# Kernel tuning notes

Measured on AMD Instinct MI355X. Metric: run time of the kernel, lower is better.

## Reference

```python
import jax, jax.numpy as jnp
import numpy as np

B, S, D = 32, 257, 1024
H, HD = 16, 64
E, R, K = 8, 16, 2
SCALE = HD ** -0.5


def _lora_linear(x, w_fixed, A_all, B_all, bias, idx, gates):
    # x: [B,S,D]; w_fixed: [O,D]; A_all: [E,R,D]; B_all: [E,O,R]; idx: [B,K]; gates: [B,K]
    base = jnp.einsum('bsd,od->bso', x, w_fixed)
    A_sel = A_all[idx]  # [B,K,R,D] per-sample expert gather
    B_sel = B_all[idx]  # [B,K,O,R]
    xa = jnp.einsum('bsd,bkrd->bksr', x, A_sel)          # low-rank down-proj
    expert = jnp.einsum('bksr,bkor,bk->bso', xa, B_sel, gates)
    return base + expert + bias


def setup_inputs() -> dict:
    key = jax.random.key(0)
    ks = jax.random.split(key, 20)
    inp = {
        'hidden_states': jax.random.normal(ks[0], (B, S, D), jnp.float32),
        'top_k_indices': jax.random.randint(ks[1], (B, K), 0, E),
        'top_k_gates': jax.random.uniform(ks[2], (B, K), jnp.float32),
    }
    i = 3
    for name in ('q', 'k', 'v', 'o'):
        inp[f'w{name}_fixed'] = jax.random.normal(ks[i], (D, D), jnp.float32) * 0.02; i += 1
        inp[f'A_{name}'] = jax.random.normal(ks[i], (E, R, D), jnp.float32) * 0.02; i += 1
        inp[f'B_{name}'] = jax.random.normal(ks[i], (E, D, R), jnp.float32) * 0.02; i += 1
        inp[f'b_{name}'] = jnp.zeros((D,), jnp.float32)
    return inp


def reference(hidden_states, top_k_indices, top_k_gates,
              wq_fixed, A_q, B_q, b_q,
              wk_fixed, A_k, B_k, b_k,
              wv_fixed, A_v, B_v, b_v,
              wo_fixed, A_o, B_o, b_o):
    idx, gates = top_k_indices, top_k_gates
    q = _lora_linear(hidden_states, wq_fixed, A_q, B_q, b_q, idx, gates) * SCALE
    k = _lora_linear(hidden_states, wk_fixed, A_k, B_k, b_k, idx, gates)
    v = _lora_linear(hidden_states, wv_fixed, A_v, B_v, b_v, idx, gates)
    # [B,S,D] -> [B,H,S,HD]
    q = q.reshape(B, S, H, HD).transpose(0, 2, 1, 3)
    k = k.reshape(B, S, H, HD).transpose(0, 2, 1, 3)
    v = v.reshape(B, S, H, HD).transpose(0, 2, 1, 3)
    attn = jax.nn.softmax(jnp.einsum('bhsd,bhtd->bhst', q, k), axis=-1)
    out = jnp.einsum('bhst,bhtd->bhsd', attn, v)
    out = out.transpose(0, 2, 1, 3).reshape(B, S, D)
    return _lora_linear(out, wo_fixed, A_o, B_o, b_o, idx, gates)
```

## Files before the change

kernel.cpp:

```cpp
#include <hip/hip_runtime.h>


#define BB 32
#define SS 257
#define DD 1024
#define HH 16
#define HDIM 64
#define EE 8
#define RR 16
#define MTOT (BB * SS)
#define MPAD 8448
#define VTS 264

typedef __attribute__((ext_vector_type(8))) _Float16 f16x8;
typedef __attribute__((ext_vector_type(4))) float f32x4;

static __device__ __forceinline__ float4 ld4(const float* p) {
    return *(const float4*)p;
}
static __device__ __forceinline__ unsigned short f16b(float x) {
    union { _Float16 f; unsigned short u; } cv;
    cv.f = (_Float16)x;
    return cv.u;
}

static __device__ __forceinline__ void gl_lds16(const unsigned short* g,
                                                unsigned short* l) {
    __builtin_amdgcn_global_load_lds(
        (const __attribute__((address_space(1))) unsigned int*)g,
        (__attribute__((address_space(3))) unsigned int*)l, 16, 0, 0);
}

static __device__ __forceinline__ int xcd_swz(int orig, int nwg) {
    const int xcd = orig & 7;
    const int lin = orig >> 3;
    const int q = nwg >> 3;
    const int r = nwg & 7;
    return (xcd < r ? xcd * (q + 1) : r * (q + 1) + (xcd - r) * q) + lin;
}

__global__ __launch_bounds__(256) void prep(
    const float* __restrict__ hidden, const float* __restrict__ wq,
    const float* __restrict__ wk, const float* __restrict__ wv,
    const float* __restrict__ wo, const float* __restrict__ Aq,
    const float* __restrict__ Ak, const float* __restrict__ Av,
    const float* __restrict__ Ao, const float* __restrict__ Bq,
    const float* __restrict__ Bk, const float* __restrict__ Bv,
    const float* __restrict__ Bo, const int* __restrict__ tki,
    const float* __restrict__ tkg, unsigned short* __restrict__ Xf,
    unsigned short* __restrict__ Wcat, unsigned short* __restrict__ Who,
    unsigned short* __restrict__ A3, unsigned short* __restrict__ Ao16,
    unsigned short* __restrict__ Bccat, unsigned short* __restrict__ Bco)
{
    const int tid = threadIdx.x;
    int bx = blockIdx.x;
    if (bx < 8448) {
        long i = ((long)bx * 256 + tid) * 4;
        float4 v = (i < (long)MTOT * DD) ? ld4(&hidden[i])
                                         : make_float4(0.f, 0.f, 0.f, 0.f);
        ushort4 hv;
        hv.x = f16b(v.x); hv.y = f16b(v.y); hv.z = f16b(v.z); hv.w = f16b(v.w);
        *(ushort4*)&Xf[i] = hv;
        return;
    }
    bx -= 8448;
    if (bx < 4096) {
        const int sel = bx >> 10;
        long i = ((long)(bx & 1023) * 256 + tid) * 4;
        const float* src = (sel == 0) ? wq : (sel == 1) ? wk
                                          : (sel == 2) ? wv : wo;
        unsigned short* dst =
            (sel < 3) ? Wcat + (size_t)sel * DD * DD : Who;
        float4 v = ld4(&src[i]);
        ushort4 hv;
        hv.x = f16b(v.x); hv.y = f16b(v.y); hv.z = f16b(v.z); hv.w = f16b(v.w);
        *(ushort4*)&dst[i] = hv;
        return;
    }
    bx -= 4096;
    if (bx < 512) {
        const int sel = bx >> 7;
        long i = ((long)(bx & 127) * 256 + tid) * 4;
        const float* src = (sel == 0) ? Aq : (sel == 1) ? Ak
                                          : (sel == 2) ? Av : Ao;
        unsigned short* dst =
            (sel < 3) ? A3 + (size_t)sel * EE * RR * DD : Ao16;
        float4 v = ld4(&src[i]);
        ushort4 hv;
        hv.x = f16b(v.x); hv.y = f16b(v.y); hv.z = f16b(v.z); hv.w = f16b(v.w);
        *(ushort4*)&dst[i] = hv;
        return;
    }
    bx -= 512;
    {
        const int set = bx >> 8;
        const int i = (bx & 255) * 256 + tid;
        const int b = i >> 11;
        const int rem = i & 2047;
        const int n = rem >> 1;
        const int ke = rem & 1;
        const float* Ball = (set == 0) ? Bq : (set == 1) ? Bk
                                           : (set == 2) ? Bv : Bo;
        const int e = tki[b * 2 + ke];
        const float g = tkg[b * 2 + ke];
        const float* sp = &Ball[((size_t)e * DD + n) * RR];
        unsigned short o16[16];
#pragma unroll
        for (int r4 = 0; r4 < 4; ++r4) {
            float4 v = ld4(sp + r4 * 4);
            o16[r4 * 4 + 0] = f16b(g * v.x);
            o16[r4 * 4 + 1] = f16b(g * v.y);
            o16[r4 * 4 + 2] = f16b(g * v.z);
            o16[r4 * 4 + 3] = f16b(g * v.w);
        }
        unsigned short* dst =
            (set < 3) ? &Bccat[((size_t)b * 3072 + set * 1024 + n) * 32 + ke * 16]
                      : &Bco[((size_t)b * 1024 + n) * 32 + ke * 16];
        *(uint4*)&dst[0] = *(uint4*)&o16[0];
        *(uint4*)&dst[8] = *(uint4*)&o16[8];
    }
}

#define XA_STAGE(BUFI, KT)                                                     \
    do {                                                                       \
        unsigned short* base_ = Sx + (BUFI) * 8192;                            \
        const int k0_ = (KT) * 32;                                             \
        gl_lds16(Xf + xr0 + k0_, base_ + lbase);                               \
        gl_lds16(Xf + xr1 + k0_, base_ + 2048 + lbase);                        \
        gl_lds16(Ap + ar0 + k0_, base_ + 4096 + lbase);                        \
        gl_lds16(Ap + ar1 + k0_, base_ + 6144 + lbase);                        \
    } while (0)

#define XA_COMPUTE(BUFI)                                                       \
    do {                                                                       \
        const unsigned short* Ab_ = Sx + (BUFI) * 8192;                        \
        const unsigned short* Bb_ = Ab_ + 4096;                                \
        f16x8 af[4], bf[4];                                                    \
        const int sb = (quad ^ ((l16 >> 1) & 3)) * 8;                          \
        _Pragma("unroll") for (int t = 0; t < 4; ++t) {                        \
            af[t] = *(const f16x8*)&Ab_[(wm + t * 16 + l16) * 32 + sb];        \
            bf[t] = *(const f16x8*)&Bb_[(wn + t * 16 + l16) * 32 + sb];        \
        }                                                                      \
        _Pragma("unroll") for (int i = 0; i < 4; ++i)                          \
        _Pragma("unroll") for (int j = 0; j < 4; ++j)                          \
            acc[i][j] = __builtin_amdgcn_mfma_f32_16x16x32_f16(                \
                af[i], bf[j], acc[i][j], 0, 0, 0);                             \
    } while (0)

#define XA_SYNC() asm volatile("s_waitcnt vmcnt(0)\n\ts_barrier" ::: "memory")

__global__ __launch_bounds__(256) void gemm_xa(
    const unsigned short* __restrict__ Xf, const unsigned short* __restrict__ A0,
    const unsigned short* __restrict__ A1, const unsigned short* __restrict__ A2,
    unsigned short* __restrict__ XA, int ncols)
{
    __shared__ unsigned short Sx[16384];
    const int tid = threadIdx.x;
    const int m0 = blockIdx.y * 128;
    const int p = blockIdx.x;
    const unsigned short* Ap = (p == 0) ? A0 : (p == 1) ? A1 : A2;
    const int lane = tid & 63;
    const int w = tid >> 6;
    const int wm = (w >> 1) * 64;
    const int wn = (w & 1) * 64;
    const int l16 = lane & 15;
    const int quad = lane >> 4;

    f32x4 acc[4][4];
#pragma unroll
    for (int i = 0; i < 4; ++i)
#pragma unroll
        for (int j = 0; j < 4; ++j) acc[i][j] = (f32x4){0.f, 0.f, 0.f, 0.f};

    const int srow = tid >> 2;
    const int scol = (((tid & 3) ^ ((tid >> 3) & 3))) * 8;
    const int lbase = (tid & 192) * 8;
    const size_t xr0 = (size_t)(m0 + srow) * DD + scol;
    const size_t xr1 = (size_t)(m0 + srow + 64) * DD + scol;
    const size_t ar0 = (size_t)srow * DD + scol;
    const size_t ar1 = (size_t)(srow + 64) * DD + scol;

    XA_STAGE(0, 0);
#pragma unroll 1
    for (int kt = 0; kt < 32; ++kt) {
        XA_SYNC();
        if (kt < 31) XA_STAGE((kt + 1) & 1, kt + 1);
        XA_COMPUTE(kt & 1);
    }

#pragma unroll
    for (int j = 0; j < 4; ++j) {
        const int col = p * 128 + wn + j * 16 + l16;
#pragma unroll
        for (int i = 0; i < 4; ++i) {
            const int mb = m0 + wm + i * 16 + quad * 4;
#pragma unroll
            for (int rg = 0; rg < 4; ++rg) {
                const int m = mb + rg;
                if (m < MTOT)
                    XA[(size_t)m * ncols + col] = f16b(acc[i][j][rg]);
            }
        }
    }
}

#define QKV_STAGE(BUFI, KT)                                                    \
    do {                                                                       \
        unsigned short* dA_ = S + (BUFI) * 16384 + w * 512;                    \
        const int k0_ = (KT) * 32;                                             \
        gl_lds16(Xf + gA + k0_, dA_);                                          \
        gl_lds16(Wcat + gB + k0_, dA_ + 8192);                                 \
    } while (0)

#define QKV_PHASES(BUFI)                                                       \
    do {                                                                       \
        const unsigned short* Ab_ = S + (BUFI) * 16384;                        \
        const unsigned short* Bb_ = Ab_ + 8192;                                \
        f16x8 af_[4], bf_[4];                                                  \
        _Pragma("unroll") for (int j = 0; j < 4; ++j)                          \
            bf_[j] = *(const f16x8*)&Bb_[boff + j * 512];                      \
        _Pragma("unroll") for (int i = 0; i < 4; ++i)                          \
            af_[i] = *(const f16x8*)&Ab_[aoff + i * 512];                      \
        __builtin_amdgcn_s_setprio(1);                                         \
        _Pragma("unroll") for (int i = 0; i < 4; ++i)                          \
        _Pragma("unroll") for (int j = 0; j < 4; ++j)                          \
            acc[i][j] = __builtin_amdgcn_mfma_f32_16x16x32_f16(                \
                af_[i], bf_[j], acc[i][j], 0, 0, 0);                           \
        __builtin_amdgcn_s_setprio(0);                                         \
    } while (0)

#define QKV_SYNC() asm volatile("s_waitcnt vmcnt(0)\n\ts_barrier" ::: "memory")

__global__ __launch_bounds__(1024)
__attribute__((amdgpu_waves_per_eu(4, 8))) void gemm_qkv(
    const unsigned short* __restrict__ Xf, const unsigned short* __restrict__ Wcat,
    const float* __restrict__ bq, const float* __restrict__ bk,
    const float* __restrict__ bv, const unsigned short* __restrict__ XAd,
    const unsigned short* __restrict__ Bccat, const int* __restrict__ idx,
    unsigned short* __restrict__ qh, unsigned short* __restrict__ kh,
    unsigned short* __restrict__ vTg)
{
    __shared__ unsigned short S[32768];
    const int tid = threadIdx.x;
    const int wgid = xcd_swz(blockIdx.x, 396);
    const int bxn = wgid % 12;
    const int m0 = (wgid / 12) * 256;
    const int p = bxn >> 2;
    const int n0g = bxn * 256;
    const int nloc0 = (bxn & 3) * 256;
    const int lane = tid & 63;
    const int w = tid >> 6;
    const int wm = (w >> 2) * 64;
    const int wn = (w & 3) * 64;
    const int l16 = lane & 15;
    const int quad = lane >> 4;
    const int sb = (quad ^ ((l16 >> 1) & 3)) * 8;
    const int aoff = (wm + l16) * 32 + sb;
    const int boff = (wn + l16) * 32 + sb;

    f32x4 acc[4][4];
#pragma unroll
    for (int i = 0; i < 4; ++i)
#pragma unroll
        for (int j = 0; j < 4; ++j) acc[i][j] = (f32x4){0.f, 0.f, 0.f, 0.f};

    const int srow = tid >> 2;
    const int schk = ((tid & 3) ^ ((srow >> 1) & 3)) * 8;
    const size_t gA = (size_t)(m0 + srow) * DD + schk;
    const size_t gB = (size_t)(n0g + srow) * DD + schk;

    QKV_STAGE(0, 0);
#pragma unroll 1
    for (int kt = 0; kt < 32; ++kt) {
        QKV_SYNC();
        if (kt < 31) QKV_STAGE((kt + 1) & 1, kt + 1);
        QKV_PHASES(kt & 1);
    }

    {
        int m_hi = m0 + 255;
        if (m_hi >= MTOT) m_hi = MTOT - 1;
        const int b_first = m0 / SS;
        const int b_last = m_hi / SS;
        const int r = tid >> 2;
        const int cc = tid & 3;
        const int key = (r >> 1) & 3;
        const int g = cc ^ key;
        const uint4 z = make_uint4(0, 0, 0, 0);
#pragma unroll 1
        for (int bp = b_first; bp <= b_last; ++bp) {
            const int gm = m0 + r;
            const bool va = (gm < MTOT) && (gm / SS == bp);
            uint4 av = z;
            if (va) {
                const int e = idx[bp * 2 + (g >> 1)];
                av = *(const uint4*)&XAd[(size_t)gm * 384 + p * 128 +
                                         e * 16 + (g & 1) * 8];
            }
            const size_t bo = ((size_t)bp * 3072 + p * 1024 + nloc0 + r) * 32;
            uint4 bv2 = *(const uint4*)&Bccat[bo + g * 8];
            __syncthreads();
            *(uint4*)&S[r * 32 + cc * 8] = av;
            *(uint4*)&S[8192 + r * 32 + cc * 8] = bv2;
            __syncthreads();
            QKV_PHASES(0);
            __syncthreads();
        }
    }

    unsigned short* Epi = S;
    const float* bias = (p == 0) ? bq : (p == 1) ? bk : bv;
    if (p < 2) {
        const float alpha = (p == 0) ? 0.125f : 1.0f;
        unsigned short* C = (p == 0) ? qh : kh;
#pragma unroll 1
        for (int qtr = 0; qtr < 4; ++qtr) {
            if ((w >> 2) == qtr) {
#pragma unroll
                for (int j = 0; j < 4; ++j) {
                    const int col = wn + j * 16 + l16;
                    const float bvl = bias[nloc0 + col];
#pragma unroll
                    for (int i = 0; i < 4; ++i) {
                        const int ml = i * 16 + quad * 4;
#pragma unroll
                        for (int rg = 0; rg < 4; ++rg)
                            Epi[(ml + rg) * 264 + col] =
                                f16b(alpha * (acc[i][j][rg] + bvl));
                    }
                }
            }
            __syncthreads();
            {
                const int r = tid >> 4;
                const int c = (tid & 15) * 16;
                const int m = m0 + qtr * 64 + r;
                if (m < MTOT) {
#pragma unroll
                    for (int k = 0; k < 2; ++k)
                        *(uint4*)&C[(size_t)m * DD + nloc0 + c + k * 8] =
                            *(const uint4*)&Epi[r * 264 + c + k * 8];
                }
            }
            __syncthreads();
        }
    } else {
#pragma unroll 1
        for (int hh = 0; hh < 4; ++hh) {
            if ((w >> 2) == hh) {
#pragma unroll
                for (int j = 0; j < 4; ++j) {
                    const int col = wn + j * 16 + l16;
                    const float bvl = bias[nloc0 + col];
#pragma unroll
                    for (int i = 0; i < 4; ++i) {
                        const int ml = i * 16 + quad * 4;
                        ushort4 pk;
                        pk.x = f16b(acc[i][j][0] + bvl);
                        pk.y = f16b(acc[i][j][1] + bvl);
                        pk.z = f16b(acc[i][j][2] + bvl);
                        pk.w = f16b(acc[i][j][3] + bvl);
                        *(ushort4*)&Epi[col * 68 + ml] = pk;
                    }
                }
            }
            __syncthreads();
            {
                const int tl = tid & 63;
                const int mg = m0 + hh * 64 + tl;
                if (mg < MTOT) {
                    const int bq2 = mg / SS;
                    const int t = mg - bq2 * SS;
#pragma unroll 4
                    for (int k = 0; k < 16; ++k) {
                        const int nll = (tid >> 6) + k * 16;
                        const int d = nloc0 + nll;
                        vTg[((size_t)(bq2 * HH + (d >> 6)) * HDIM + (d & 63)) *
                                VTS + t] = Epi[nll * 68 + tl];
                    }
                }
            }
            __syncthreads();
        }
    }
}

#define O_STAGE(BUFI, KT)                                                      \
    do {                                                                       \
        unsigned short* b_ = S + (BUFI) * 12288;                               \
        const int k0_ = (KT) * 32;                                             \
        gl_lds16(Xf + gA1 + k0_, b_ + w * 1024);                               \
        gl_lds16(Xf + gA2 + k0_, b_ + w * 1024 + 512);                         \
        gl_lds16(Wh2 + gB + k0_, b_ + 8192 + w * 512);                         \
    } while (0)

#define O_PHASES(BUFI)                                                         \
    do {                                                                       \
        const unsigned short* Ab_ = S + (BUFI) * 12288;                        \
        const unsigned short* Bb_ = Ab_ + 8192;                                \
        f16x8 af_[4], bf_[4];                                                  \
        _Pragma("unroll") for (int j = 0; j < 4; ++j)                          \
            bf_[j] = *(const f16x8*)&Bb_[boff + j * 512];                      \
        _Pragma("unroll") for (int i = 0; i < 4; ++i)                          \
            af_[i] = *(const f16x8*)&Ab_[aoff + i * 512];                      \
        __builtin_amdgcn_s_setprio(1);                                         \
        _Pragma("unroll") for (int i = 0; i < 4; ++i)                          \
        _Pragma("unroll") for (int j = 0; j < 4; ++j)                          \
            acc[i][j] = __builtin_amdgcn_mfma_f32_16x16x32_f16(                \
                af_[i], bf_[j], acc[i][j], 0, 0, 0);                           \
        __builtin_amdgcn_s_setprio(0);                                         \
    } while (0)

__global__ __launch_bounds__(512)
__attribute__((amdgpu_waves_per_eu(2, 8))) void gemm_o(
    const unsigned short* __restrict__ Xf, const unsigned short* __restrict__ Wh2,
    const float* __restrict__ bias, const unsigned short* __restrict__ XAo,
    const unsigned short* __restrict__ Bco, const int* __restrict__ idx,
    float* __restrict__ Cf)
{
    __shared__ unsigned short S[24576];
    const int tid = threadIdx.x;
    const int wgid = xcd_swz(blockIdx.x, 264);
    const int m0 = (wgid >> 3) * 256;
    const int n0 = (wgid & 7) * 128;
    const int lane = tid & 63;
    const int w = tid >> 6;
    const int wm = (w >> 1) * 64;
    const int wn = (w & 1) * 64;
    const int l16 = lane & 15;
    const int quad = lane >> 4;
    const int sb = (quad ^ ((l16 >> 1) & 3)) * 8;
    const int aoff = (wm + l16) * 32 + sb;
    const int boff = (wn + l16) * 32 + sb;

    f32x4 acc[4][4];
#pragma unroll
    for (int i = 0; i < 4; ++i)
#pragma unroll
        for (int j = 0; j < 4; ++j) acc[i][j] = (f32x4){0.f, 0.f, 0.f, 0.f};

    const int rowA1 = w * 32 + (lane >> 2);
    const int chk = lane & 3;
    const int keyA = (rowA1 >> 1) & 3;
    const size_t gA1 = (size_t)(m0 + rowA1) * DD + (chk ^ keyA) * 8;
    const size_t gA2 = gA1 + (size_t)16 * DD;
    const int rowB = w * 16 + (lane >> 2);
    const int keyB = (rowB >> 1) & 3;
    const size_t gB = (size_t)(n0 + rowB) * DD + (chk ^ keyB) * 8;

    O_STAGE(0, 0);
#pragma unroll 1
    for (int kt = 0; kt < 32; ++kt) {
        QKV_SYNC();
        if (kt < 31) O_STAGE((kt + 1) & 1, kt + 1);
        O_PHASES(kt & 1);
    }

    {
        int m_hi = m0 + 255;
        if (m_hi >= MTOT) m_hi = MTOT - 1;
        const int b_first = m0 / SS;
        const int b_last = m_hi / SS;
        const int rA = tid >> 1;
        const int b0 = (tid & 1) * 2;
        const int keyTA = (rA >> 1) & 3;
        const int g0 = b0 ^ keyTA, g1 = (b0 + 1) ^ keyTA;
        const int rB = tid >> 2;
        const int ccB = tid & 3;
        const int gBt = ccB ^ ((rB >> 1) & 3);
        const uint4 z = make_uint4(0, 0, 0, 0);
#pragma unroll 1
        for (int bp = b_first; bp <= b_last; ++bp) {
            const int gm = m0 + rA;
            const bool va = (gm < MTOT) && (gm / SS == bp);
            uint4 av0 = z, av1 = z;
            if (va) {
                const int e0 = idx[bp * 2 + (g0 >> 1)];
                const int e1 = idx[bp * 2 + (g1 >> 1)];
                av0 = *(const uint4*)&XAo[(size_t)gm * 128 + e0 * 16 +
                                          (g0 & 1) * 8];
                av1 = *(const uint4*)&XAo[(size_t)gm * 128 + e1 * 16 +
                                          (g1 & 1) * 8];
            }
            const size_t bo = ((size_t)bp * 1024 + n0 + rB) * 32;
            uint4 bv2 = *(const uint4*)&Bco[bo + gBt * 8];
            __syncthreads();
            *(uint4*)&S[rA * 32 + b0 * 8] = av0;
            *(uint4*)&S[rA * 32 + (b0 + 1) * 8] = av1;
            *(uint4*)&S[8192 + rB * 32 + ccB * 8] = bv2;
            __syncthreads();
            O_PHASES(0);
            __syncthreads();
        }
    }

#pragma unroll
    for (int j = 0; j < 4; ++j) {
        const int n = n0 + wn + j * 16 + l16;
        const float bvl = bias[n];
#pragma unroll
        for (int i = 0; i < 4; ++i) {
            const int mb = m0 + wm + i * 16 + quad * 4;
#pragma unroll
            for (int rg = 0; rg < 4; ++rg) {
                const int m = mb + rg;
                if (m < MTOT) Cf[(size_t)m * DD + n] = acc[i][j][rg] + bvl;
            }
        }
    }
}

__global__ __launch_bounds__(512, 1) void attn_v4(
    const unsigned short* __restrict__ qh, const unsigned short* __restrict__ kh,
    const unsigned short* __restrict__ vT, unsigned short* __restrict__ Xf)
{
    __shared__ unsigned short Ks[288 * 64];
    __shared__ unsigned short Vt[64 * VTS];
    __shared__ unsigned short Qs[64 * 64];
    __shared__ unsigned short Ps[64 * 296];
    __shared__ float sredm[2][64];
    __shared__ float sreds[2][64];

    const int tid = threadIdx.x;
    const int h = blockIdx.x, b = blockIdx.y;
    const int cb = h * HDIM;
    const int lane = tid & 63;
    const int w = tid >> 6;
    const int r0 = (w & 3) * 16;
    const int ch = w >> 2;
    const int l16 = lane & 15;
    const int quad = lane >> 4;

    const size_t kbase = (size_t)(b * SS) * DD + cb;
    {
        const int rr = w * 8 + (lane >> 3);
        const int cg = ((lane & 7) ^ (rr & 7)) * 8;
#pragma unroll
        for (int c = 0; c < 4; ++c)
            gl_lds16(kh + kbase + (size_t)(c * 64 + rr) * DD + cg,
                     &Ks[(c * 64 + w * 8) * 64]);
    }
    if (tid < 256) {
        uint4 z = make_uint4(0, 0, 0, 0);
        if (tid < 8) z = *(const uint4*)&kh[kbase + (size_t)256 * DD + tid * 8];
        *(uint4*)&Ks[256 * 64 + tid * 8] = z;
    }
    {
        const size_t vbase = (size_t)(b * HH + h) * HDIM * VTS;
        for (int i = tid; i < 64 * 33; i += 512) {
            const int r = i / 33;
            const int c = i - r * 33;
            uint4 v = *(const uint4*)&vT[vbase + (size_t)r * VTS + c * 8];
            if (c == 32) { v.x &= 0xFFFFu; v.y = 0; v.z = 0; v.w = 0; }
            *(uint4*)&Vt[r * VTS + c * 8] = v;
        }
    }

#pragma unroll 1
    for (int qt = 0; qt < 5; ++qt) {
        const int s0 = qt * 64;
        __syncthreads();
        {
            int sg = s0 + (tid >> 3);
            if (sg > SS - 1) sg = SS - 1;
            const int cg = ((tid & 7) ^ ((tid >> 3) & 7)) * 8;
            gl_lds16(qh + (size_t)(b * SS + sg) * DD + cb + cg,
                     &Qs[(w * 8) * 64]);
        }
        __syncthreads();

        f32x4 lac[9];
#pragma unroll
        for (int ct = 0; ct < 9; ++ct) lac[ct] = (f32x4){0.f, 0.f, 0.f, 0.f};
#pragma unroll
        for (int kc = 0; kc < 2; ++kc) {
            const int sb = ((kc * 4 + quad) ^ (l16 & 7)) * 8;
            f16x8 af = *(const f16x8*)&Qs[(r0 + l16) * 64 + sb];
#pragma unroll
            for (int ct = 0; ct < 9; ++ct) {
                const int c0 = ch * 144 + ct * 16;
                f16x8 bf = *(const f16x8*)&Ks[(c0 + l16) * 64 + sb];
                lac[ct] = __builtin_amdgcn_mfma_f32_16x16x32_f16(
                    af, bf, lac[ct], 0, 0, 0);
            }
        }
#pragma unroll
        for (int ct = 0; ct < 9; ++ct) {
            const int t = ch * 144 + ct * 16 + l16;
            if (t > SS - 1) {
                lac[ct][0] = -1e30f; lac[ct][1] = -1e30f;
                lac[ct][2] = -1e30f; lac[ct][3] = -1e30f;
            }
        }
        float mx[4] = {-1e30f, -1e30f, -1e30f, -1e30f};
#pragma unroll
        for (int ct = 0; ct < 9; ++ct)
#pragma unroll
            for (int i = 0; i < 4; ++i) mx[i] = fmaxf(mx[i], lac[ct][i]);
#pragma unroll
        for (int o = 1; o < 16; o <<= 1)
#pragma unroll
            for (int i = 0; i < 4; ++i)
                mx[i] = fmaxf(mx[i], __shfl_xor(mx[i], o, 16));
        if (l16 == 0)
#pragma unroll
            for (int i = 0; i < 4; ++i) sredm[ch][r0 + quad * 4 + i] = mx[i];
        __syncthreads();
#pragma unroll
        for (int i = 0; i < 4; ++i)
            mx[i] = fmaxf(mx[i], sredm[1 - ch][r0 + quad * 4 + i]);
        float sm[4] = {0.f, 0.f, 0.f, 0.f};
#pragma unroll
        for (int ct = 0; ct < 9; ++ct)
#pragma unroll
            for (int i = 0; i < 4; ++i) {
                float pv = __expf(lac[ct][i] - mx[i]);
                lac[ct][i] = pv;
                sm[i] += pv;
            }
#pragma unroll
        for (int o = 1; o < 16; o <<= 1)
#pragma unroll
            for (int i = 0; i < 4; ++i) sm[i] += __shfl_xor(sm[i], o, 16);
        if (l16 == 0)
#pragma unroll
            for (int i = 0; i < 4; ++i) sreds[ch][r0 + quad * 4 + i] = sm[i];
        __syncthreads();
        float inv[4];
#pragma unroll
        for (int i = 0; i < 4; ++i)
            inv[i] = 1.f / (sm[i] + sreds[1 - ch][r0 + quad * 4 + i]);
#pragma unroll
        for (int ct = 0; ct < 9; ++ct) {
            const int col = ch * 144 + ct * 16 + l16;
#pragma unroll
            for (int i = 0; i < 4; ++i)
                Ps[(r0 + quad * 4 + i) * 296 + col] =
                    f16b(lac[ct][i] * inv[i]);
        }
        __syncthreads();

        f32x4 oacc[2];
        oacc[0] = (f32x4){0.f, 0.f, 0.f, 0.f};
        oacc[1] = (f32x4){0.f, 0.f, 0.f, 0.f};
#pragma unroll
        for (int tt = 0; tt < 9; ++tt) {
            const int t0 = tt * 32;
            f16x8 pf = *(const f16x8*)&Ps[(r0 + l16) * 296 + t0 + quad * 8];
#pragma unroll
            for (int dt = 0; dt < 2; ++dt) {
                f16x8 bvv = *(const f16x8*)&Vt[(ch * 32 + dt * 16 + l16) * VTS +
                                               t0 + quad * 8];
                oacc[dt] = __builtin_amdgcn_mfma_f32_16x16x32_f16(
                    pf, bvv, oacc[dt], 0, 0, 0);
            }
        }
#pragma unroll
        for (int dt = 0; dt < 2; ++dt)
#pragma unroll
            for (int i = 0; i < 4; ++i) {
                const int srow = s0 + r0 + quad * 4 + i;
                if (srow < SS)
                    Xf[(size_t)(b * SS + srow) * DD + cb + ch * 32 + dt * 16 +
                       l16] = f16b(oacc[dt][i]);
            }
    }
}

extern "C" void kernel_launch(void* const* d_in, const int* in_sizes, int n_in,
                              void* d_out, int out_size, void* d_ws,
                              size_t ws_size, hipStream_t stream)
{
    const float* hidden = (const float*)d_in[0];
    const int* tki = (const int*)d_in[1];
    const float* tkg = (const float*)d_in[2];
    const float* wq = (const float*)d_in[3];
    const float* Aq = (const float*)d_in[4];
    const float* Bq = (const float*)d_in[5];
    const float* bq = (const float*)d_in[6];
    const float* wk = (const float*)d_in[7];
    const float* Ak = (const float*)d_in[8];
    const float* Bk = (const float*)d_in[9];
    const float* bkb = (const float*)d_in[10];
    const float* wv = (const float*)d_in[11];
    const float* Av = (const float*)d_in[12];
    const float* Bv = (const float*)d_in[13];
    const float* bvb = (const float*)d_in[14];
    const float* wo = (const float*)d_in[15];
    const float* Ao = (const float*)d_in[16];
    const float* Bo = (const float*)d_in[17];
    const float* bob = (const float*)d_in[18];
    float* out = (float*)d_out;

    char* ws = (char*)d_ws;
    const size_t NW = (size_t)DD * DD;
    const size_t NA = (size_t)EE * RR * DD;
    unsigned short* Xf = (unsigned short*)ws;    ws += (size_t)MPAD * DD * 2;
    unsigned short* qh = (unsigned short*)ws;    ws += (size_t)MTOT * DD * 2;
    unsigned short* vTg = (unsigned short*)ws;   ws += (size_t)BB * HH * HDIM * VTS * 2;
    unsigned short* Wcat = (unsigned short*)ws;  ws += 3 * NW * 2;
    unsigned short* Who = (unsigned short*)ws;   ws += NW * 2;
    unsigned short* A3 = (unsigned short*)ws;    ws += 3 * NA * 2;
    unsigned short* Ao16 = (unsigned short*)ws;  ws += NA * 2;
    unsigned short* Bccat = (unsigned short*)ws; ws += (size_t)BB * 3072 * 32 * 2;
    unsigned short* Bco = (unsigned short*)ws;   ws += (size_t)BB * 1024 * 32 * 2;
    unsigned short* XAo = (unsigned short*)ws;   ws += (size_t)MTOT * 128 * 2;
    unsigned short* kh = (unsigned short*)d_out;
    unsigned short* XAd = (unsigned short*)((char*)d_out + (size_t)MTOT * DD * 2);

    prep<<<14080, 256, 0, stream>>>(hidden, wq, wk, wv, wo, Aq, Ak, Av, Ao,
                                    Bq, Bk, Bv, Bo, tki, tkg, Xf, Wcat, Who,
                                    A3, Ao16, Bccat, Bco);
    gemm_xa<<<dim3(3, 65), 256, 0, stream>>>(Xf, A3, A3 + NA, A3 + 2 * NA,
                                             XAd, 384);
    gemm_qkv<<<396, 1024, 0, stream>>>(Xf, Wcat, bq, bkb, bvb, XAd,
                                       Bccat, tki, qh, kh, vTg);
    attn_v4<<<dim3(HH, BB), 512, 0, stream>>>(qh, kh, vTg, Xf);
    gemm_xa<<<dim3(1, 65), 256, 0, stream>>>(Xf, Ao16, Ao16, Ao16, XAo, 128);
    gemm_o<<<264, 512, 0, stream>>>(Xf, Who, bob, XAo, Bco, tki, out);
}
```

Measured before the change: 324.8 us.

## Retile QKV GEMM to 256x128 tiles with 512-thread blocks reusing O-GEMM pipeline

```diff
diff --git a/kernel.cpp b/kernel.cpp
--- a/kernel.cpp
+++ b/kernel.cpp
@@ -121,6 +121,8 @@
     }
 }
 
+#define GSYNC() asm volatile("s_waitcnt vmcnt(0)\n\ts_barrier" ::: "memory")
+
 #define XA_STAGE(BUFI, KT)                                                     \
     do {                                                                       \
         unsigned short* base_ = Sx + (BUFI) * 8192;                            \
@@ -146,8 +148,6 @@
             acc[i][j] = __builtin_amdgcn_mfma_f32_16x16x32_f16(                \
                 af[i], bf[j], acc[i][j], 0, 0, 0);                             \
     } while (0)
-
-#define XA_SYNC() asm volatile("s_waitcnt vmcnt(0)\n\ts_barrier" ::: "memory")
 
 __global__ __launch_bounds__(256) void gemm_xa(
     const unsigned short* __restrict__ Xf, const unsigned short* __restrict__ A0,
@@ -183,7 +183,7 @@
     XA_STAGE(0, 0);
 #pragma unroll 1
     for (int kt = 0; kt < 32; ++kt) {
-        XA_SYNC();
+        GSYNC();
         if (kt < 31) XA_STAGE((kt + 1) & 1, kt + 1);
         XA_COMPUTE(kt & 1);
     }
@@ -204,197 +204,16 @@
     }
 }
 
-#define QKV_STAGE(BUFI, KT)                                                    \
-    do {                                                                       \
-        unsigned short* dA_ = S + (BUFI) * 16384 + w * 512;                    \
-        const int k0_ = (KT) * 32;                                             \
-        gl_lds16(Xf + gA + k0_, dA_);                                          \
-        gl_lds16(Wcat + gB + k0_, dA_ + 8192);                                 \
-    } while (0)
-
-#define QKV_PHASES(BUFI)                                                       \
-    do {                                                                       \
-        const unsigned short* Ab_ = S + (BUFI) * 16384;                        \
-        const unsigned short* Bb_ = Ab_ + 8192;                                \
-        f16x8 af_[4], bf_[4];                                                  \
-        _Pragma("unroll") for (int j = 0; j < 4; ++j)                          \
-            bf_[j] = *(const f16x8*)&Bb_[boff + j * 512];                      \
-        _Pragma("unroll") for (int i = 0; i < 4; ++i)                          \
-            af_[i] = *(const f16x8*)&Ab_[aoff + i * 512];                      \
-        __builtin_amdgcn_s_setprio(1);                                         \
-        _Pragma("unroll") for (int i = 0; i < 4; ++i)                          \
-        _Pragma("unroll") for (int j = 0; j < 4; ++j)                          \
-            acc[i][j] = __builtin_amdgcn_mfma_f32_16x16x32_f16(                \
-                af_[i], bf_[j], acc[i][j], 0, 0, 0);                           \
-        __builtin_amdgcn_s_setprio(0);                                         \
-    } while (0)
-
-#define QKV_SYNC() asm volatile("s_waitcnt vmcnt(0)\n\ts_barrier" ::: "memory")
-
-__global__ __launch_bounds__(1024)
-__attribute__((amdgpu_waves_per_eu(4, 8))) void gemm_qkv(
-    const unsigned short* __restrict__ Xf, const unsigned short* __restrict__ Wcat,
-    const float* __restrict__ bq, const float* __restrict__ bk,
-    const float* __restrict__ bv, const unsigned short* __restrict__ XAd,
-    const unsigned short* __restrict__ Bccat, const int* __restrict__ idx,
-    unsigned short* __restrict__ qh, unsigned short* __restrict__ kh,
-    unsigned short* __restrict__ vTg)
-{
-    __shared__ unsigned short S[32768];
-    const int tid = threadIdx.x;
-    const int wgid = xcd_swz(blockIdx.x, 396);
-    const int bxn = wgid % 12;
-    const int m0 = (wgid / 12) * 256;
-    const int p = bxn >> 2;
-    const int n0g = bxn * 256;
-    const int nloc0 = (bxn & 3) * 256;
-    const int lane = tid & 63;
-    const int w = tid >> 6;
-    const int wm = (w >> 2) * 64;
-    const int wn = (w & 3) * 64;
-    const int l16 = lane & 15;
-    const int quad = lane >> 4;
-    const int sb = (quad ^ ((l16 >> 1) & 3)) * 8;
-    const int aoff = (wm + l16) * 32 + sb;
-    const int boff = (wn + l16) * 32 + sb;
-
-    f32x4 acc[4][4];
-#pragma unroll
-    for (int i = 0; i < 4; ++i)
-#pragma unroll
-        for (int j = 0; j < 4; ++j) acc[i][j] = (f32x4){0.f, 0.f, 0.f, 0.f};
-
-    const int srow = tid >> 2;
-    const int schk = ((tid & 3) ^ ((srow >> 1) & 3)) * 8;
-    const size_t gA = (size_t)(m0 + srow) * DD + schk;
-    const size_t gB = (size_t)(n0g + srow) * DD + schk;
-
-    QKV_STAGE(0, 0);
-#pragma unroll 1
-    for (int kt = 0; kt < 32; ++kt) {
-        QKV_SYNC();
-        if (kt < 31) QKV_STAGE((kt + 1) & 1, kt + 1);
-        QKV_PHASES(kt & 1);
-    }
-
-    {
-        int m_hi = m0 + 255;
-        if (m_hi >= MTOT) m_hi = MTOT - 1;
-        const int b_first = m0 / SS;
-        const int b_last = m_hi / SS;
-        const int r = tid >> 2;
-        const int cc = tid & 3;
-        const int key = (r >> 1) & 3;
-        const int g = cc ^ key;
-        const uint4 z = make_uint4(0, 0, 0, 0);
-#pragma unroll 1
-        for (int bp = b_first; bp <= b_last; ++bp) {
-            const int gm = m0 + r;
-            const bool va = (gm < MTOT) && (gm / SS == bp);
-            uint4 av = z;
-            if (va) {
-                const int e = idx[bp * 2 + (g >> 1)];
-                av = *(const uint4*)&XAd[(size_t)gm * 384 + p * 128 +
-                                         e * 16 + (g & 1) * 8];
-            }
-            const size_t bo = ((size_t)bp * 3072 + p * 1024 + nloc0 + r) * 32;
-            uint4 bv2 = *(const uint4*)&Bccat[bo + g * 8];
-            __syncthreads();
-            *(uint4*)&S[r * 32 + cc * 8] = av;
-            *(uint4*)&S[8192 + r * 32 + cc * 8] = bv2;
-            __syncthreads();
-            QKV_PHASES(0);
-            __syncthreads();
-        }
-    }
-
-    unsigned short* Epi = S;
-    const float* bias = (p == 0) ? bq : (p == 1) ? bk : bv;
-    if (p < 2) {
-        const float alpha = (p == 0) ? 0.125f : 1.0f;
-        unsigned short* C = (p == 0) ? qh : kh;
-#pragma unroll 1
-        for (int qtr = 0; qtr < 4; ++qtr) {
-            if ((w >> 2) == qtr) {
-#pragma unroll
-                for (int j = 0; j < 4; ++j) {
-                    const int col = wn + j * 16 + l16;
-                    const float bvl = bias[nloc0 + col];
-#pragma unroll
-                    for (int i = 0; i < 4; ++i) {
-                        const int ml = i * 16 + quad * 4;
-#pragma unroll
-                        for (int rg = 0; rg < 4; ++rg)
-                            Epi[(ml + rg) * 264 + col] =
-                                f16b(alpha * (acc[i][j][rg] + bvl));
-                    }
-                }
-            }
-            __syncthreads();
-            {
-                const int r = tid >> 4;
-                const int c = (tid & 15) * 16;
-                const int m = m0 + qtr * 64 + r;
-                if (m < MTOT) {
-#pragma unroll
-                    for (int k = 0; k < 2; ++k)
-                        *(uint4*)&C[(size_t)m * DD + nloc0 + c + k * 8] =
-                            *(const uint4*)&Epi[r * 264 + c + k * 8];
-                }
-            }
-            __syncthreads();
-        }
-    } else {
-#pragma unroll 1
-        for (int hh = 0; hh < 4; ++hh) {
-            if ((w >> 2) == hh) {
-#pragma unroll
-                for (int j = 0; j < 4; ++j) {
-                    const int col = wn + j * 16 + l16;
-                    const float bvl = bias[nloc0 + col];
-#pragma unroll
-                    for (int i = 0; i < 4; ++i) {
-                        const int ml = i * 16 + quad * 4;
-                        ushort4 pk;
-                        pk.x = f16b(acc[i][j][0] + bvl);
-                        pk.y = f16b(acc[i][j][1] + bvl);
-                        pk.z = f16b(acc[i][j][2] + bvl);
-                        pk.w = f16b(acc[i][j][3] + bvl);
-                        *(ushort4*)&Epi[col * 68 + ml] = pk;
-                    }
-                }
-            }
-            __syncthreads();
-            {
-                const int tl = tid & 63;
-                const int mg = m0 + hh * 64 + tl;
-                if (mg < MTOT) {
-                    const int bq2 = mg / SS;
-                    const int t = mg - bq2 * SS;
-#pragma unroll 4
-                    for (int k = 0; k < 16; ++k) {
-                        const int nll = (tid >> 6) + k * 16;
-                        const int d = nloc0 + nll;
-                        vTg[((size_t)(bq2 * HH + (d >> 6)) * HDIM + (d & 63)) *
-                                VTS + t] = Epi[nll * 68 + tl];
-                    }
-                }
-            }
-            __syncthreads();
-        }
-    }
-}
-
-#define O_STAGE(BUFI, KT)                                                      \
+#define T3_STAGE(BUFI, KT, BMAT)                                               \
     do {                                                                       \
         unsigned short* b_ = S + (BUFI) * 12288;                               \
         const int k0_ = (KT) * 32;                                             \
         gl_lds16(Xf + gA1 + k0_, b_ + w * 1024);                               \
         gl_lds16(Xf + gA2 + k0_, b_ + w * 1024 + 512);                         \
-        gl_lds16(Wh2 + gB + k0_, b_ + 8192 + w * 512);                         \
+        gl_lds16(BMAT + gB + k0_, b_ + 8192 + w * 512);                        \
     } while (0)
 
-#define O_PHASES(BUFI)                                                         \
+#define T3_PHASES(BUFI)                                                        \
     do {                                                                       \
         const unsigned short* Ab_ = S + (BUFI) * 12288;                        \
         const unsigned short* Bb_ = Ab_ + 8192;                                \
@@ -410,6 +229,172 @@
                 af_[i], bf_[j], acc[i][j], 0, 0, 0);                           \
         __builtin_amdgcn_s_setprio(0);                                         \
     } while (0)
+
+__global__ __launch_bounds__(512)
+__attribute__((amdgpu_waves_per_eu(2, 8))) void gemm_qkv(
+    const unsigned short* __restrict__ Xf, const unsigned short* __restrict__ Wcat,
+    const float* __restrict__ bq, const float* __restrict__ bk,
+    const float* __restrict__ bv, const unsigned short* __restrict__ XAd,
+    const unsigned short* __restrict__ Bccat, const int* __restrict__ idx,
+    unsigned short* __restrict__ qh, unsigned short* __restrict__ kh,
+    unsigned short* __restrict__ vTg)
+{
+    __shared__ unsigned short S[24576];
+    const int tid = threadIdx.x;
+    const int wgid = xcd_swz(blockIdx.x, 792);
+    const int bxn = wgid % 24;
+    const int m0 = (wgid / 24) * 256;
+    const int p = bxn >> 3;
+    const int n0g = bxn * 128;
+    const int nloc0 = (bxn & 7) * 128;
+    const int lane = tid & 63;
+    const int w = tid >> 6;
+    const int wm = (w >> 1) * 64;
+    const int wn = (w & 1) * 64;
+    const int l16 = lane & 15;
+    const int quad = lane >> 4;
+    const int sb = (quad ^ ((l16 >> 1) & 3)) * 8;
+    const int aoff = (wm + l16) * 32 + sb;
+    const int boff = (wn + l16) * 32 + sb;
+
+    f32x4 acc[4][4];
+#pragma unroll
+    for (int i = 0; i < 4; ++i)
+#pragma unroll
+        for (int j = 0; j < 4; ++j) acc[i][j] = (f32x4){0.f, 0.f, 0.f, 0.f};
+
+    const int rowA1 = w * 32 + (lane >> 2);
+    const int chk = lane & 3;
+    const int keyA = (rowA1 >> 1) & 3;
+    const size_t gA1 = (size_t)(m0 + rowA1) * DD + (chk ^ keyA) * 8;
+    const size_t gA2 = gA1 + (size_t)16 * DD;
+    const int rowB = w * 16 + (lane >> 2);
+    const int keyB = (rowB >> 1) & 3;
+    const size_t gB = (size_t)(n0g + rowB) * DD + (chk ^ keyB) * 8;
+
+    T3_STAGE(0, 0, Wcat);
+#pragma unroll 1
+    for (int kt = 0; kt < 32; ++kt) {
+        GSYNC();
+        if (kt < 31) T3_STAGE((kt + 1) & 1, kt + 1, Wcat);
+        T3_PHASES(kt & 1);
+    }
+
+    {
+        int m_hi = m0 + 255;
+        if (m_hi >= MTOT) m_hi = MTOT - 1;
+        const int b_first = m0 / SS;
+        const int b_last = m_hi / SS;
+        const int rA = tid >> 1;
+        const int b0 = (tid & 1) * 2;
+        const int keyTA = (rA >> 1) & 3;
+        const int g0 = b0 ^ keyTA, g1 = (b0 + 1) ^ keyTA;
+        const int rB = tid >> 2;
+        const int ccB = tid & 3;
+        const int gBt = ccB ^ ((rB >> 1) & 3);
+        const uint4 z = make_uint4(0, 0, 0, 0);
+#pragma unroll 1
+        for (int bp = b_first; bp <= b_last; ++bp) {
+            const int gm = m0 + rA;
+            const bool va = (gm < MTOT) && (gm / SS == bp);
+            uint4 av0 = z, av1 = z;
+            if (va) {
+                const int e0 = idx[bp * 2 + (g0 >> 1)];
+                const int e1 = idx[bp * 2 + (g1 >> 1)];
+                av0 = *(const uint4*)&XAd[(size_t)gm * 384 + p * 128 +
+                                          e0 * 16 + (g0 & 1) * 8];
+                av1 = *(const uint4*)&XAd[(size_t)gm * 384 + p * 128 +
+                                          e1 * 16 + (g1 & 1) * 8];
+            }
+            const size_t bo = ((size_t)bp * 3072 + p * 1024 + nloc0 + rB) * 32;
+            uint4 bv2 = *(const uint4*)&Bccat[bo + gBt * 8];
+            __syncthreads();
+            *(uint4*)&S[rA * 32 + b0 * 8] = av0;
+            *(uint4*)&S[rA * 32 + (b0 + 1) * 8] = av1;
+            *(uint4*)&S[8192 + rB * 32 + ccB * 8] = bv2;
+            __syncthreads();
+            T3_PHASES(0);
+            __syncthreads();
+        }
+    }
+
+    unsigned short* Epi = S;
+    const float* bias = (p == 0) ? bq : (p == 1) ? bk : bv;
+    if (p < 2) {
+        const float alpha = (p == 0) ? 0.125f : 1.0f;
+        unsigned short* C = (p == 0) ? qh : kh;
+#pragma unroll 1
+        for (int half = 0; half < 2; ++half) {
+            if ((w >> 2) == half) {
+                const int lm0 = wm - half * 128;
+#pragma unroll
+                for (int j = 0; j < 4; ++j) {
+                    const int col = wn + j * 16 + l16;
+                    const float bvl = bias[nloc0 + col];
+#pragma unroll
+                    for (int i = 0; i < 4; ++i) {
+                        const int ml = lm0 + i * 16 + quad * 4;
+#pragma unroll
+                        for (int rg = 0; rg < 4; ++rg)
+                            Epi[(ml + rg) * 136 + col] =
+                                f16b(alpha * (acc[i][j][rg] + bvl));
+                    }
+                }
+            }
+            __syncthreads();
+            {
+                const int r = tid >> 2;
+                const int c = (tid & 3) * 32;
+                const int m = m0 + half * 128 + r;
+                if (m < MTOT) {
+#pragma unroll
+                    for (int k = 0; k < 4; ++k)
+                        *(uint4*)&C[(size_t)m * DD + nloc0 + c + k * 8] =
+                            *(const uint4*)&Epi[r * 136 + c + k * 8];
+                }
+            }
+            __syncthreads();
+        }
+    } else {
+#pragma unroll 1
+        for (int hh = 0; hh < 4; ++hh) {
+            if ((w >> 1) == hh) {
+#pragma unroll
+                for (int j = 0; j < 4; ++j) {
+                    const int col = wn + j * 16 + l16;
+                    const float bvl = bias[nloc0 + col];
+#pragma unroll
+                    for (int i = 0; i < 4; ++i) {
+                        const int ml = i * 16 + quad * 4;
+                        ushort4 pk;
+                        pk.x = f16b(acc[i][j][0] + bvl);
+                        pk.y = f16b(acc[i][j][1] + bvl);
+                        pk.z = f16b(acc[i][j][2] + bvl);
+                        pk.w = f16b(acc[i][j][3] + bvl);
+                        *(ushort4*)&Epi[col * 68 + ml] = pk;
+                    }
+                }
+            }
+            __syncthreads();
+            {
+                const int tl = tid & 63;
+                const int mg = m0 + hh * 64 + tl;
+                if (mg < MTOT) {
+                    const int bq2 = mg / SS;
+                    const int t = mg - bq2 * SS;
+#pragma unroll 4
+                    for (int k = 0; k < 16; ++k) {
+                        const int nll = (tid >> 6) + k * 8;
+                        const int d = nloc0 + nll;
+                        vTg[((size_t)(bq2 * HH + (d >> 6)) * HDIM + (d & 63)) *
+                                VTS + t] = Epi[nll * 68 + tl];
+                    }
+                }
+            }
+            __syncthreads();
+        }
+    }
+}
 
 __global__ __launch_bounds__(512)
 __attribute__((amdgpu_waves_per_eu(2, 8))) void gemm_o(
@@ -448,12 +433,12 @@
     const int keyB = (rowB >> 1) & 3;
     const size_t gB = (size_t)(n0 + rowB) * DD + (chk ^ keyB) * 8;
 
-    O_STAGE(0, 0);
+    T3_STAGE(0, 0, Wh2);
 #pragma unroll 1
     for (int kt = 0; kt < 32; ++kt) {
-        QKV_SYNC();
-        if (kt < 31) O_STAGE((kt + 1) & 1, kt + 1);
-        O_PHASES(kt & 1);
+        GSYNC();
+        if (kt < 31) T3_STAGE((kt + 1) & 1, kt + 1, Wh2);
+        T3_PHASES(kt & 1);
     }
 
     {
@@ -489,7 +474,7 @@
             *(uint4*)&S[rA * 32 + (b0 + 1) * 8] = av1;
             *(uint4*)&S[8192 + rB * 32 + ccB * 8] = bv2;
             __syncthreads();
-            O_PHASES(0);
+            T3_PHASES(0);
             __syncthreads();
         }
     }
@@ -713,8 +698,8 @@
                                     A3, Ao16, Bccat, Bco);
     gemm_xa<<<dim3(3, 65), 256, 0, stream>>>(Xf, A3, A3 + NA, A3 + 2 * NA,
                                              XAd, 384);
-    gemm_qkv<<<396, 1024, 0, stream>>>(Xf, Wcat, bq, bkb, bvb, XAd,
-                                       Bccat, tki, qh, kh, vTg);
+    gemm_qkv<<<792, 512, 0, stream>>>(Xf, Wcat, bq, bkb, bvb, XAd,
+                                      Bccat, tki, qh, kh, vTg);
     attn_v4<<<dim3(HH, BB), 512, 0, stream>>>(qh, kh, vTg, Xf);
     gemm_xa<<<dim3(1, 65), 256, 0, stream>>>(Xf, Ao16, Ao16, Ao16, XAo, 128);
     gemm_o<<<264, 512, 0, stream>>>(Xf, Who, bob, XAo, Bco, tki, out);
```

Result: slower. 358.9 us (+10.5%).
